# Performance work log

Measured on AMD Instinct MI355X. Metric: run time of the kernel, lower is better.

The kernel has to match this reference:

```python
import jax, jax.numpy as jnp
import numpy as np

N_HEADS = 16

def _rel_emb(table, len_q, len_k):
    # table: [2P+1, d] -> [len_q, len_k, d] via clipped relative distance lookup
    P = (table.shape[0] - 1) // 2
    rel = jnp.arange(len_k)[None, :] - jnp.arange(len_q)[:, None]
    idx = jnp.clip(rel, -P, P) + P
    return table[idx]

def setup_inputs() -> dict:
    key = jax.random.key(0)
    ks = jax.random.split(key, 13)
    B, S, E = 2, 2048, 1024
    P = 128
    d = E // N_HEADS
    s = 0.02
    return {
        "q": jax.random.normal(ks[0], (B, S, E), jnp.float32),
        "k": jax.random.normal(ks[1], (B, S, E), jnp.float32),
        "v": jax.random.normal(ks[2], (B, S, E), jnp.float32),
        "Wq": jax.random.normal(ks[3], (E, E), jnp.float32) * s,
        "bq": jnp.zeros((E,), jnp.float32),
        "Wk": jax.random.normal(ks[4], (E, E), jnp.float32) * s,
        "bk": jnp.zeros((E,), jnp.float32),
        "Wv": jax.random.normal(ks[5], (E, E), jnp.float32) * s,
        "bv": jnp.zeros((E,), jnp.float32),
        "Wo": jax.random.normal(ks[6], (E, E), jnp.float32) * s,
        "bo": jnp.zeros((E,), jnp.float32),
        "rk_table": jax.random.normal(ks[7], (2 * P + 1, d), jnp.float32) * s,
        "rv_table": jax.random.normal(ks[8], (2 * P + 1, d), jnp.float32) * s,
    }

def reference(q, k, v, Wq, bq, Wk, bk, Wv, bv, Wo, bo, rk_table, rv_table):
    B, Sq, E = q.shape
    Sk = k.shape[1]
    H = N_HEADS
    d = E // H
    scale = jnp.sqrt(jnp.asarray(d, q.dtype))

    qh = (q @ Wq.T + bq).reshape(B, Sq, H, d).transpose(0, 2, 1, 3)  # [B,H,Sq,d]
    kh = (k @ Wk.T + bk).reshape(B, Sk, H, d).transpose(0, 2, 1, 3)
    vh = (v @ Wv.T + bv).reshape(B, Sk, H, d).transpose(0, 2, 1, 3)

    qk = jnp.einsum('bhqd,bhkd->bhqk', qh, kh)
    r_k = _rel_emb(rk_table, Sq, Sk)                 # [Sq,Sk,d]
    q_rk = jnp.einsum('bhqd,qkd->bhqk', qh, r_k)
    attn = jax.nn.softmax((qk + q_rk) / scale, axis=-1)  # dropout p=0

    w1 = jnp.einsum('bhqk,bhkd->bhqd', attn, vh)
    r_v = _rel_emb(rv_table, Sq, Sk)
    w2 = jnp.einsum('bhqk,qkd->bhqd', attn, r_v)

    out = (w1 + w2).transpose(0, 2, 1, 3).reshape(B, Sq, E)
    return out @ Wo.T + bo
```

## Files before the change

### kernel.cpp

```cpp
#include <hip/hip_runtime.h>
#include <hip/hip_bf16.h>
#include <cstdint>
#include <cstddef>

#define NH   16
#define DH   64
#define SQ   2048
#define NB   2
#define EM   1024
#define NREL 257
#define QSTR 258
#define SCL  0.18033688f
#define NR   ((size_t)NB * NH * SQ)

typedef unsigned short ushort_t;
using bf16x8 = __attribute__((ext_vector_type(8))) __bf16;
using bf16x4 = __attribute__((ext_vector_type(4))) __bf16;
using f32x4  = __attribute__((ext_vector_type(4))) float;
#define MFMA16(a, b, c) __builtin_amdgcn_mfma_f32_16x16x32_bf16(a, b, c, 0, 0, 0)

__device__ __forceinline__ ushort_t f2bf(float f) {
    union { __bf16 h; ushort_t u; } x; x.h = (__bf16)f; return x.u;
}
__device__ __forceinline__ float bf2f(ushort_t u) {
    union { unsigned u; float f; } x; x.u = ((unsigned)u) << 16;
    return x.f;
}
__device__ __forceinline__ uint2 pack4(float a, float b, float c, float d) {
    union { bf16x4 v; uint2 u; } x;
    x.v = (bf16x4){ (__bf16)a, (__bf16)b, (__bf16)c, (__bf16)d };
    return x.u;
}
__device__ __forceinline__ int kperm(int x) {
    return (x & ~63) | ((x & 15) << 2) | ((x >> 4) & 3);
}
__device__ __forceinline__ void gl_lds16(const void* g, void* l) {
    __builtin_amdgcn_global_load_lds(
        (const __attribute__((address_space(1))) unsigned int*)g,
        (__attribute__((address_space(3))) unsigned int*)l, 16, 0, 0);
}

__global__ __launch_bounds__(256)
void cvt3(const float* __restrict__ a, const float* __restrict__ b,
          const float* __restrict__ c, ushort_t* __restrict__ oa,
          ushort_t* __restrict__ ob, ushort_t* __restrict__ oc, int n)
{
    const float* in = blockIdx.y == 0 ? a : (blockIdx.y == 1 ? b : c);
    ushort_t* out   = blockIdx.y == 0 ? oa : (blockIdx.y == 1 ? ob : oc);
    int i = (blockIdx.x * 256 + threadIdx.x) * 8;
    if (i < n) {
        float4 v0 = *reinterpret_cast<const float4*>(in + i);
        float4 v1 = *reinterpret_cast<const float4*>(in + i + 4);
        uint2 lo = pack4(v0.x, v0.y, v0.z, v0.w);
        uint2 hi = pack4(v1.x, v1.y, v1.z, v1.w);
        *reinterpret_cast<uint4*>(out + i) = make_uint4(lo.x, lo.y, hi.x, hi.y);
    }
}
__global__ __launch_bounds__(256)
void cvt4(const float* __restrict__ a, const float* __restrict__ b,
          const float* __restrict__ c, const float* __restrict__ d,
          ushort_t* __restrict__ oa, ushort_t* __restrict__ ob,
          ushort_t* __restrict__ oc, ushort_t* __restrict__ od, int n)
{
    const float* in = blockIdx.y == 0 ? a : (blockIdx.y == 1 ? b :
                      (blockIdx.y == 2 ? c : d));
    ushort_t* out   = blockIdx.y == 0 ? oa : (blockIdx.y == 1 ? ob :
                      (blockIdx.y == 2 ? oc : od));
    int i = (blockIdx.x * 256 + threadIdx.x) * 8;
    if (i < n) {
        float4 v0 = *reinterpret_cast<const float4*>(in + i);
        float4 v1 = *reinterpret_cast<const float4*>(in + i + 4);
        uint2 lo = pack4(v0.x, v0.y, v0.z, v0.w);
        uint2 hi = pack4(v1.x, v1.y, v1.z, v1.w);
        *reinterpret_cast<uint4*>(out + i) = make_uint4(lo.x, lo.y, hi.x, hi.y);
    }
}

__global__ __launch_bounds__(256)
void prep_tables(const float* __restrict__ rv, const float* __restrict__ rk,
                 ushort_t* __restrict__ rvT, ushort_t* __restrict__ rkb)
{
    int idx = blockIdx.x * 256 + threadIdx.x;
    if (idx < 64 * 256) {
        int d = idx >> 8, c = idx & 255;
        rvT[d * 256 + kperm(c)] = f2bf(rv[(size_t)(c + 1) * DH + d]);
    }
    idx -= 64 * 256;
    if (idx >= 0 && idx < 272 * 64) {
        int j = idx >> 6, d2 = idx & 63;
        rkb[idx] = (j < NREL) ? f2bf(rk[(size_t)j * DH + d2]) : (ushort_t)0;
    }
}

template<int MODE>
__global__ __launch_bounds__(256)
void gemm_bt(const ushort_t* __restrict__ A, const ushort_t* __restrict__ W,
             const float* __restrict__ bias, void* __restrict__ dstv,
             int M, int N, int K)
{
    __shared__ ushort_t As[128 * 32];
    __shared__ ushort_t Bs[128 * 32];
    const int t = threadIdx.x, lane = t & 63;
    const int wv = t >> 6, wr = wv >> 1, wc = wv & 1;
    const int g = lane >> 4, c16 = lane & 15;
    const int rowi = lane >> 2, chi = lane & 3;

    const int nwg = gridDim.x * gridDim.y;
    int flat = blockIdx.y * gridDim.x + blockIdx.x;
    int rm = (flat & 7) * (nwg >> 3) + (flat >> 3);
    const int n0 = (rm % gridDim.x) * 128;
    const int m0 = (rm / gridDim.x) * 128;

    f32x4 acc[4][4];
#pragma unroll
    for (int i = 0; i < 4; ++i)
#pragma unroll
        for (int j = 0; j < 4; ++j) acc[i][j] = (f32x4){0.f, 0.f, 0.f, 0.f};

    for (int k0 = 0; k0 < K; k0 += 32) {
        __syncthreads();
#pragma unroll
        for (int j = 0; j < 2; ++j) {
            const int rbase = wv * 32 + j * 16;
            gl_lds16(A + (size_t)(m0 + rbase + rowi) * K + k0 + chi * 8,
                     As + rbase * 32);
            gl_lds16(W + (size_t)(n0 + rbase + rowi) * K + k0 + chi * 8,
                     Bs + rbase * 32);
        }
        __syncthreads();

        bf16x8 af[4], bfr[4];
#pragma unroll
        for (int i = 0; i < 4; ++i)
            af[i] = *reinterpret_cast<const bf16x8*>(As + (wr * 64 + i * 16 + c16) * 32 + g * 8);
#pragma unroll
        for (int j = 0; j < 4; ++j)
            bfr[j] = *reinterpret_cast<const bf16x8*>(Bs + (wc * 64 + j * 16 + c16) * 32 + g * 8);
#pragma unroll
        for (int i = 0; i < 4; ++i)
#pragma unroll
            for (int j = 0; j < 4; ++j)
                acc[i][j] = MFMA16(af[i], bfr[j], acc[i][j]);
    }

#pragma unroll
    for (int j = 0; j < 4; ++j) {
        const int n = n0 + wc * 64 + j * 16 + c16;
        const float bn = bias[n];
#pragma unroll
        for (int i = 0; i < 4; ++i) {
#pragma unroll
            for (int r = 0; r < 4; ++r) {
                const int m = m0 + wr * 64 + i * 16 + 4 * g + r;
                const float vv = acc[i][j][r] + bn;
                if (MODE == 0) {
                    ((float*)dstv)[(size_t)m * N + n] = vv;
                } else {
                    const int b = m >> 11, s = m & (SQ - 1);
                    const int h = n >> 6, dd = n & 63;
                    if (MODE == 1) {
                        ((ushort_t*)dstv)[(((size_t)b * NH + h) * SQ + s) * DH + dd] = f2bf(vv);
                    } else {
                        const int sp = kperm(s);
                        ((ushort_t*)dstv)[(((size_t)b * NH + h) * DH + dd) * SQ + sp] = f2bf(vv);
                    }
                }
            }
        }
    }
}

__global__ __launch_bounds__(256)
void qrel_mfma(const ushort_t* __restrict__ qh, const ushort_t* __restrict__ rkb,
               ushort_t* __restrict__ qrel)
{
    const int t = threadIdx.x, lane = t & 63, w = t >> 6;
    const int g = lane >> 4, c16 = lane & 15;
    const size_t r0 = (size_t)blockIdx.x * 64 + w * 16;

    bf16x8 af[2];
#pragma unroll
    for (int ks = 0; ks < 2; ++ks)
        af[ks] = *reinterpret_cast<const bf16x8*>(qh + (r0 + c16) * DH + ks * 32 + g * 8);

    f32x4 acc[17];
#pragma unroll
    for (int n = 0; n < 17; ++n) acc[n] = (f32x4){0.f, 0.f, 0.f, 0.f};
#pragma unroll
    for (int n = 0; n < 17; ++n)
#pragma unroll
        for (int ks = 0; ks < 2; ++ks) {
            bf16x8 bf = *reinterpret_cast<const bf16x8*>(
                rkb + (size_t)(16 * n + c16) * DH + ks * 32 + g * 8);
            acc[n] = MFMA16(af[ks], bf, acc[n]);
        }
#pragma unroll
    for (int n = 0; n < 17; ++n) {
        const int j = 16 * n + c16;
        if (j < NREL) {
#pragma unroll
            for (int r = 0; r < 4; ++r)
                qrel[(r0 + 4 * g + r) * QSTR + j] = f2bf(acc[n][r] * SCL);
        }
    }
}

__global__ __launch_bounds__(256, 4)
void attn_flash(const ushort_t* __restrict__ qh, const ushort_t* __restrict__ kh,
                const ushort_t* __restrict__ vt, const ushort_t* __restrict__ qrel,
                ushort_t* __restrict__ Ptile, float* __restrict__ w1g,
                float* __restrict__ lacg, float* __restrict__ b0g,
                float* __restrict__ b256g)
{
    __shared__ ushort_t Ks[64 * 72];
    __shared__ ushort_t Vs[64 * 72];
    __shared__ ushort_t PQs[64 * 72];

    const int t = threadIdx.x, lane = t & 63, w = t >> 6;
    const int g = lane >> 4, c16 = lane & 15;
    const int nwg = gridDim.x * gridDim.y;
    int flat = blockIdx.y * gridDim.x + blockIdx.x;
    int rmid = (flat & 7) * (nwg >> 3) + (flat >> 3);
    const int q0 = (rmid & 31) * 64;
    const int bh = rmid >> 5;
    const size_t Gbase = ((size_t)bh * 32 + (q0 >> 6)) * 5;

#pragma unroll
    for (int l = 0; l < 2; ++l) {
        const int fid = t + 256 * l;
        const int row = fid >> 3, ch = fid & 7;
        uint4 v = *reinterpret_cast<const uint4*>(
            qh + ((size_t)bh * SQ + q0 + row) * DH + ch * 8);
        *reinterpret_cast<uint4*>(PQs + row * 72 + ch * 8) = v;
    }
    __syncthreads();
    bf16x8 qf[2];
#pragma unroll
    for (int ks = 0; ks < 2; ++ks)
        qf[ks] = *reinterpret_cast<const bf16x8*>(PQs + (w * 16 + c16) * 72 + ks * 32 + g * 8);

    const ushort_t* qrb = qrel + ((size_t)bh * SQ + q0) * QSTR;
    float q0add[4], q256add[4];
#pragma unroll
    for (int i = 0; i < 4; ++i) {
        const int r = w * 16 + 4 * g + i;
        q0add[i]   = bf2f(qrb[(size_t)r * QSTR + 0]);
        q256add[i] = bf2f(qrb[(size_t)r * QSTR + 256]);
    }

    f32x4 w1[4];
#pragma unroll
    for (int n = 0; n < 4; ++n) w1[n] = (f32x4){0.f, 0.f, 0.f, 0.f};
    float lac[4] = {0.f,0.f,0.f,0.f}, b0[4] = {0.f,0.f,0.f,0.f}, b256[4] = {0.f,0.f,0.f,0.f};

    const int row_l = t >> 3, ch_l = t & 7;
    const int row_h = row_l + 32;
    uint4 kr0, kr1, vr0, vr1;
    {
        kr0 = *reinterpret_cast<const uint4*>(kh + ((size_t)bh * SQ + row_l) * DH + ch_l * 8);
        kr1 = *reinterpret_cast<const uint4*>(kh + ((size_t)bh * SQ + row_h) * DH + ch_l * 8);
        vr0 = *reinterpret_cast<const uint4*>(vt + ((size_t)bh * DH + row_l) * SQ + ch_l * 8);
        vr1 = *reinterpret_cast<const uint4*>(vt + ((size_t)bh * DH + row_h) * SQ + ch_l * 8);
    }

    for (int k0 = 0; k0 < SQ; k0 += 64) {
        __syncthreads();
        *reinterpret_cast<uint4*>(Ks + row_l * 72 + ch_l * 8) = kr0;
        *reinterpret_cast<uint4*>(Ks + row_h * 72 + ch_l * 8) = kr1;
        *reinterpret_cast<uint4*>(Vs + row_l * 72 + ch_l * 8) = vr0;
        *reinterpret_cast<uint4*>(Vs + row_h * 72 + ch_l * 8) = vr1;
        __syncthreads();
        if (k0 + 64 < SQ) {
            kr0 = *reinterpret_cast<const uint4*>(kh + ((size_t)bh * SQ + k0 + 64 + row_l) * DH + ch_l * 8);
            kr1 = *reinterpret_cast<const uint4*>(kh + ((size_t)bh * SQ + k0 + 64 + row_h) * DH + ch_l * 8);
            vr0 = *reinterpret_cast<const uint4*>(vt + ((size_t)bh * DH + row_l) * SQ + k0 + 64 + ch_l * 8);
            vr1 = *reinterpret_cast<const uint4*>(vt + ((size_t)bh * DH + row_h) * SQ + k0 + 64 + ch_l * 8);
        }

        f32x4 s[4];
#pragma unroll
        for (int n = 0; n < 4; ++n) s[n] = (f32x4){0.f, 0.f, 0.f, 0.f};
        __builtin_amdgcn_s_setprio(1);
#pragma unroll
        for (int ks = 0; ks < 2; ++ks)
#pragma unroll
            for (int n = 0; n < 4; ++n) {
                bf16x8 kf = *reinterpret_cast<const bf16x8*>(
                    Ks + (16 * n + c16) * 72 + ks * 32 + g * 8);
                s[n] = MFMA16(qf[ks], kf, s[n]);
            }
        __builtin_amdgcn_s_setprio(0);

        const int rel0 = k0 - q0;
        float rsum[4] = {0.f, 0.f, 0.f, 0.f};
        if (rel0 <= -192 || rel0 >= 192) {
            const bool lo = rel0 < 0;
#pragma unroll
            for (int i = 0; i < 4; ++i) {
                const float add = lo ? q0add[i] : q256add[i];
#pragma unroll
                for (int n = 0; n < 4; ++n) {
                    const float p = exp2f(fmaf(s[n][i], SCL, add));
                    s[n][i] = p; rsum[i] += p;
                }
                if (lo) b0[i] += rsum[i]; else b256[i] += rsum[i];
                const int qloc = w * 16 + 4 * g + i;
                *reinterpret_cast<uint2*>(PQs + qloc * 72 + c16 * 4) =
                    pack4(s[0][i], s[1][i], s[2][i], s[3][i]);
            }
        } else if (rel0 == -128 || rel0 == 128) {
            const int tix = (rel0 + 128) >> 6;
#pragma unroll
            for (int i = 0; i < 4; ++i) {
                const int qloc = w * 16 + 4 * g + i;
                const ushort_t* qrow = qrb + (size_t)qloc * QSTR;
                float z[4];
#pragma unroll
                for (int n = 0; n < 4; ++n) {
                    const int rel = rel0 + 16 * n + c16 - qloc;
                    const int idx = rel < -128 ? 0 : (rel > 128 ? 256 : rel + 128);
                    const float p = exp2f(fmaf(s[n][i], SCL, bf2f(qrow[idx])));
                    s[n][i] = p; rsum[i] += p;
                    const bool inb = (rel >= -127) & (rel <= 127);
                    z[n] = inb ? p : 0.f;
                    if (rel <= -128)      b0[i] += p;
                    else if (rel >= 128)  b256[i] += p;
                }
                *reinterpret_cast<uint2*>(PQs + qloc * 72 + c16 * 4) =
                    pack4(s[0][i], s[1][i], s[2][i], s[3][i]);
                *reinterpret_cast<uint2*>(
                    Ptile + ((Gbase + tix) * 64 + qloc) * 64 + 4 * c16) =
                    pack4(z[0], z[1], z[2], z[3]);
            }
        } else {
            const int tix = (rel0 + 128) >> 6;
#pragma unroll
            for (int i = 0; i < 4; ++i) {
                const int qloc = w * 16 + 4 * g + i;
                const ushort_t* qrow = qrb + (size_t)qloc * QSTR;
#pragma unroll
                for (int n = 0; n < 4; ++n) {
                    const int rel = rel0 + 16 * n + c16 - qloc;
                    const float p = exp2f(fmaf(s[n][i], SCL, bf2f(qrow[rel + 128])));
                    s[n][i] = p; rsum[i] += p;
                }
                const uint2 pk = pack4(s[0][i], s[1][i], s[2][i], s[3][i]);
                *reinterpret_cast<uint2*>(PQs + qloc * 72 + c16 * 4) = pk;
                *reinterpret_cast<uint2*>(
                    Ptile + ((Gbase + tix) * 64 + qloc) * 64 + 4 * c16) = pk;
            }
        }
#pragma unroll
        for (int i = 0; i < 4; ++i) lac[i] += rsum[i];

        __builtin_amdgcn_s_setprio(1);
#pragma unroll
        for (int ks = 0; ks < 2; ++ks) {
            bf16x8 pf = *reinterpret_cast<const bf16x8*>(
                PQs + (w * 16 + c16) * 72 + ks * 32 + g * 8);
#pragma unroll
            for (int n = 0; n < 4; ++n) {
                bf16x8 vf = *reinterpret_cast<const bf16x8*>(
                    Vs + (16 * n + c16) * 72 + ks * 32 + g * 8);
                w1[n] = MFMA16(pf, vf, w1[n]);
            }
        }
        __builtin_amdgcn_s_setprio(0);
    }

#pragma unroll
    for (int m = 1; m < 16; m <<= 1)
#pragma unroll
        for (int i = 0; i < 4; ++i) {
            lac[i]  += __shfl_xor(lac[i],  m, 64);
            b0[i]   += __shfl_xor(b0[i],   m, 64);
            b256[i] += __shfl_xor(b256[i], m, 64);
        }
    if (c16 == 0) {
#pragma unroll
        for (int i = 0; i < 4; ++i) {
            const size_t row = (size_t)bh * SQ + q0 + w * 16 + 4 * g + i;
            lacg[row] = lac[i]; b0g[row] = b0[i]; b256g[row] = b256[i];
        }
    }
#pragma unroll
    for (int n = 0; n < 4; ++n)
#pragma unroll
        for (int i = 0; i < 4; ++i) {
            const size_t row = (size_t)bh * SQ + q0 + w * 16 + 4 * g + i;
            w1g[row * DH + 16 * n + c16] = w1[n][i];
        }
}

__global__ __launch_bounds__(256)
void band_gemm(const ushort_t* __restrict__ Ptile, const ushort_t* __restrict__ rvT,
               const float* __restrict__ rv_f32, const float* __restrict__ w1g,
               const float* __restrict__ lacg, const float* __restrict__ b0g,
               const float* __restrict__ b256g, ushort_t* __restrict__ wout)
{
    __shared__ ushort_t Pband[64 * 264];
    const int t = threadIdx.x, lane = t & 63, w = t >> 6;
    const int g = lane >> 4, c16 = lane & 15;
    const int G = blockIdx.x;
    const size_t r0 = (size_t)G * 64;
    const int q0 = (G & 31) * 64;

    for (int i = t; i < 64 * 264 / 2; i += 256)
        reinterpret_cast<unsigned*>(Pband)[i] = 0u;
    __syncthreads();

    for (int u = t; u < 5 * 64 * 16; u += 256) {
        const int tix = u >> 10;
        const int kt0 = q0 + (tix - 2) * 64;
        if (kt0 < 0 || kt0 >= SQ) continue;
        const int qloc = (u >> 4) & 63;
        const int c = u & 15;
        uint2 pv = *reinterpret_cast<const uint2*>(
            Ptile + (((size_t)G * 5 + tix) * 64 + qloc) * 64 + 4 * c);
        const ushort_t* pe = reinterpret_cast<const ushort_t*>(&pv);
        const int relbase = (tix - 2) * 64 - qloc + 127;
#pragma unroll
        for (int n = 0; n < 4; ++n) {
            const int x = relbase + 16 * n + c;
            if (x >= 0 && x <= 254)
                Pband[qloc * 264 + ((x & ~63) | ((x & 15) << 2) | ((x >> 4) & 3))] = pe[n];
        }
    }
    if (t < 64) Pband[t * 264 + 255] = f2bf(b256g[r0 + t]);
    __syncthreads();

    f32x4 acc[4];
#pragma unroll
    for (int n = 0; n < 4; ++n) acc[n] = (f32x4){0.f, 0.f, 0.f, 0.f};
#pragma unroll
    for (int ks = 0; ks < 8; ++ks) {
        bf16x8 pm = *reinterpret_cast<const bf16x8*>(
            Pband + (w * 16 + c16) * 264 + ks * 32 + g * 8);
#pragma unroll
        for (int n = 0; n < 4; ++n) {
            bf16x8 rf = *reinterpret_cast<const bf16x8*>(
                rvT + (size_t)(16 * n + c16) * 256 + ks * 32 + g * 8);
            acc[n] = MFMA16(pm, rf, acc[n]);
        }
    }

#pragma unroll
    for (int i = 0; i < 4; ++i) {
        const size_t row = r0 + w * 16 + 4 * g + i;
        const float inv = 1.0f / lacg[row];
        const float vb0 = b0g[row];
        const int b = (int)(row >> 15), h = (int)((row >> 11) & 15), s = (int)(row & 2047);
#pragma unroll
        for (int n = 0; n < 4; ++n) {
            const int col = 16 * n + c16;
            const float val = (w1g[row * DH + col] + acc[n][i] + vb0 * rv_f32[col]) * inv;
            wout[(((size_t)b * SQ + s) * NH + h) * DH + col] = f2bf(val);
        }
    }
}

extern "C" void kernel_launch(void* const* d_in, const int* in_sizes, int n_in,
                              void* d_out, int out_size, void* d_ws, size_t ws_size,
                              hipStream_t stream)
{
    const float* q  = (const float*)d_in[0];
    const float* k  = (const float*)d_in[1];
    const float* v  = (const float*)d_in[2];
    const float* Wq = (const float*)d_in[3];
    const float* bq = (const float*)d_in[4];
    const float* Wk = (const float*)d_in[5];
    const float* bk = (const float*)d_in[6];
    const float* Wv = (const float*)d_in[7];
    const float* bv = (const float*)d_in[8];
    const float* Wo = (const float*)d_in[9];
    const float* bo = (const float*)d_in[10];
    const float* rk = (const float*)d_in[11];
    const float* rv = (const float*)d_in[12];

    char* ws = (char*)d_ws;
    auto alloc = [&](size_t bytes) { char* p = ws; ws += bytes; return p; };
    const size_t QB = (size_t)NB * SQ * EM * 2;
    const size_t WB = (size_t)EM * EM * 2;

    char* region0 = alloc(NR * 320 * 2);
    ushort_t* Ptile = (ushort_t*)region0;
    ushort_t* qbf = (ushort_t*)region0;
    ushort_t* kbf = (ushort_t*)(region0 + QB);
    ushort_t* vbf = (ushort_t*)(region0 + 2 * QB);
    ushort_t* Wqb = (ushort_t*)(region0 + 3 * QB);
    ushort_t* Wkb = (ushort_t*)(region0 + 3 * QB + WB);
    ushort_t* Wvb = (ushort_t*)(region0 + 3 * QB + 2 * WB);

    ushort_t* Wob  = (ushort_t*)alloc(WB);
    ushort_t* qhb  = (ushort_t*)alloc(QB);
    ushort_t* khb  = (ushort_t*)alloc(QB);
    ushort_t* vtb  = (ushort_t*)alloc(QB);
    ushort_t* wbuf = (ushort_t*)alloc(QB);
    ushort_t* rvT  = (ushort_t*)alloc(64 * 256 * 2);
    ushort_t* rkb  = (ushort_t*)alloc(272 * 64 * 2);
    ushort_t* qrel = (ushort_t*)alloc(NR * QSTR * 2);
    float*    w1g  = (float*)alloc(NR * DH * 4);
    float*    lacg = (float*)alloc(NR * 4);
    float*    b0g  = (float*)alloc(NR * 4);
    float*    b256g= (float*)alloc(NR * 4);

    const int NQ = NB * SQ * EM;
    const int NW = EM * EM;
    cvt3<<<dim3(NQ / 2048, 3), 256, 0, stream>>>(q, k, v, qbf, kbf, vbf, NQ);
    cvt4<<<dim3(NW / 2048, 4), 256, 0, stream>>>(Wq, Wk, Wv, Wo, Wqb, Wkb, Wvb, Wob, NW);
    prep_tables<<<132, 256, 0, stream>>>(rv, rk, rvT, rkb);

    const int M = NB * SQ;
    dim3 gg(EM / 128, M / 128);
    gemm_bt<1><<<gg, 256, 0, stream>>>(qbf, Wqb, bq, qhb, M, EM, EM);
    gemm_bt<1><<<gg, 256, 0, stream>>>(kbf, Wkb, bk, khb, M, EM, EM);
    gemm_bt<2><<<gg, 256, 0, stream>>>(vbf, Wvb, bv, vtb, M, EM, EM);
    qrel_mfma<<<(int)(NR / 64), 256, 0, stream>>>(qhb, rkb, qrel);

    attn_flash<<<dim3(32, 32), 256, 0, stream>>>(qhb, khb, vtb, qrel,
                                                 Ptile, w1g, lacg, b0g, b256g);
    band_gemm<<<(int)(NR / 64), 256, 0, stream>>>(Ptile, rvT, rv, w1g, lacg,
                                                  b0g, b256g, wbuf);
    gemm_bt<0><<<gg, 256, 0, stream>>>(wbuf, Wob, bo, d_out, M, EM, EM);
}
```

Before: 282.5 us.

## Fuse band GEMM epilogue into flash attention and halve GEMM N-tile

The relative-value band GEMM and the final normalization now run inside the attention kernel, reusing its shared memory for the band tile. The w1, row-sum and boundary-sum values stay in registers instead of going to global memory and being read back by a separate kernel, which also saves a launch. The projection GEMMs switch from 128x128 to 128x64 tiles, doubling the grid to improve CU fill. In exchange, attention blocks need more LDS and registers, which may reduce occupancy, and the smaller GEMM tiles reuse each loaded A tile less.

```diff
diff --git a/kernel.cpp b/kernel.cpp
--- a/kernel.cpp
+++ b/kernel.cpp
@@ -99,7 +99,7 @@
              int M, int N, int K)
 {
     __shared__ ushort_t As[128 * 32];
-    __shared__ ushort_t Bs[128 * 32];
+    __shared__ ushort_t Bs[64 * 32];
     const int t = threadIdx.x, lane = t & 63;
     const int wv = t >> 6, wr = wv >> 1, wc = wv & 1;
     const int g = lane >> 4, c16 = lane & 15;
@@ -108,14 +108,14 @@
     const int nwg = gridDim.x * gridDim.y;
     int flat = blockIdx.y * gridDim.x + blockIdx.x;
     int rm = (flat & 7) * (nwg >> 3) + (flat >> 3);
-    const int n0 = (rm % gridDim.x) * 128;
+    const int n0 = (rm % gridDim.x) * 64;
     const int m0 = (rm / gridDim.x) * 128;
 
-    f32x4 acc[4][4];
+    f32x4 acc[4][2];
 #pragma unroll
     for (int i = 0; i < 4; ++i)
 #pragma unroll
-        for (int j = 0; j < 4; ++j) acc[i][j] = (f32x4){0.f, 0.f, 0.f, 0.f};
+        for (int j = 0; j < 2; ++j) acc[i][j] = (f32x4){0.f, 0.f, 0.f, 0.f};
 
     for (int k0 = 0; k0 < K; k0 += 32) {
         __syncthreads();
@@ -124,28 +124,31 @@
             const int rbase = wv * 32 + j * 16;
             gl_lds16(A + (size_t)(m0 + rbase + rowi) * K + k0 + chi * 8,
                      As + rbase * 32);
+        }
+        {
+            const int rbase = wv * 16;
             gl_lds16(W + (size_t)(n0 + rbase + rowi) * K + k0 + chi * 8,
                      Bs + rbase * 32);
         }
         __syncthreads();
 
-        bf16x8 af[4], bfr[4];
+        bf16x8 af[4], bfr[2];
 #pragma unroll
         for (int i = 0; i < 4; ++i)
             af[i] = *reinterpret_cast<const bf16x8*>(As + (wr * 64 + i * 16 + c16) * 32 + g * 8);
 #pragma unroll
-        for (int j = 0; j < 4; ++j)
-            bfr[j] = *reinterpret_cast<const bf16x8*>(Bs + (wc * 64 + j * 16 + c16) * 32 + g * 8);
+        for (int j = 0; j < 2; ++j)
+            bfr[j] = *reinterpret_cast<const bf16x8*>(Bs + (wc * 32 + j * 16 + c16) * 32 + g * 8);
 #pragma unroll
         for (int i = 0; i < 4; ++i)
 #pragma unroll
-            for (int j = 0; j < 4; ++j)
+            for (int j = 0; j < 2; ++j)
                 acc[i][j] = MFMA16(af[i], bfr[j], acc[i][j]);
     }
 
 #pragma unroll
-    for (int j = 0; j < 4; ++j) {
-        const int n = n0 + wc * 64 + j * 16 + c16;
+    for (int j = 0; j < 2; ++j) {
+        const int n = n0 + wc * 32 + j * 16 + c16;
         const float bn = bias[n];
 #pragma unroll
         for (int i = 0; i < 4; ++i) {
@@ -208,13 +211,14 @@
 __global__ __launch_bounds__(256, 4)
 void attn_flash(const ushort_t* __restrict__ qh, const ushort_t* __restrict__ kh,
                 const ushort_t* __restrict__ vt, const ushort_t* __restrict__ qrel,
-                ushort_t* __restrict__ Ptile, float* __restrict__ w1g,
-                float* __restrict__ lacg, float* __restrict__ b0g,
-                float* __restrict__ b256g)
-{
-    __shared__ ushort_t Ks[64 * 72];
-    __shared__ ushort_t Vs[64 * 72];
-    __shared__ ushort_t PQs[64 * 72];
+                const ushort_t* __restrict__ rvT, const float* __restrict__ rv_f32,
+                ushort_t* __restrict__ Ptile, ushort_t* __restrict__ wout)
+{
+    __shared__ ushort_t SM[64 * 264];
+    ushort_t* Ks  = SM;
+    ushort_t* Vs  = SM + 4608;
+    ushort_t* PQs = SM + 9216;
+    ushort_t* Pband = SM;
 
     const int t = threadIdx.x, lane = t & 63, w = t >> 6;
     const int g = lane >> 4, c16 = lane & 15;
@@ -223,7 +227,7 @@
     int rmid = (flat & 7) * (nwg >> 3) + (flat >> 3);
     const int q0 = (rmid & 31) * 64;
     const int bh = rmid >> 5;
-    const size_t Gbase = ((size_t)bh * 32 + (q0 >> 6)) * 5;
+    const size_t Gbase = (size_t)rmid * 5;
 
 #pragma unroll
     for (int l = 0; l < 2; ++l) {
@@ -376,35 +380,8 @@
             b0[i]   += __shfl_xor(b0[i],   m, 64);
             b256[i] += __shfl_xor(b256[i], m, 64);
         }
-    if (c16 == 0) {
-#pragma unroll
-        for (int i = 0; i < 4; ++i) {
-            const size_t row = (size_t)bh * SQ + q0 + w * 16 + 4 * g + i;
-            lacg[row] = lac[i]; b0g[row] = b0[i]; b256g[row] = b256[i];
-        }
-    }
-#pragma unroll
-    for (int n = 0; n < 4; ++n)
-#pragma unroll
-        for (int i = 0; i < 4; ++i) {
-            const size_t row = (size_t)bh * SQ + q0 + w * 16 + 4 * g + i;
-            w1g[row * DH + 16 * n + c16] = w1[n][i];
-        }
-}
-
-__global__ __launch_bounds__(256)
-void band_gemm(const ushort_t* __restrict__ Ptile, const ushort_t* __restrict__ rvT,
-               const float* __restrict__ rv_f32, const float* __restrict__ w1g,
-               const float* __restrict__ lacg, const float* __restrict__ b0g,
-               const float* __restrict__ b256g, ushort_t* __restrict__ wout)
-{
-    __shared__ ushort_t Pband[64 * 264];
-    const int t = threadIdx.x, lane = t & 63, w = t >> 6;
-    const int g = lane >> 4, c16 = lane & 15;
-    const int G = blockIdx.x;
-    const size_t r0 = (size_t)G * 64;
-    const int q0 = (G & 31) * 64;
-
+
+    __syncthreads();
     for (int i = t; i < 64 * 264 / 2; i += 256)
         reinterpret_cast<unsigned*>(Pband)[i] = 0u;
     __syncthreads();
@@ -416,7 +393,7 @@
         const int qloc = (u >> 4) & 63;
         const int c = u & 15;
         uint2 pv = *reinterpret_cast<const uint2*>(
-            Ptile + (((size_t)G * 5 + tix) * 64 + qloc) * 64 + 4 * c);
+            Ptile + ((Gbase + tix) * 64 + qloc) * 64 + 4 * c);
         const ushort_t* pe = reinterpret_cast<const ushort_t*>(&pv);
         const int relbase = (tix - 2) * 64 - qloc + 127;
 #pragma unroll
@@ -426,12 +403,16 @@
                 Pband[qloc * 264 + ((x & ~63) | ((x & 15) << 2) | ((x >> 4) & 3))] = pe[n];
         }
     }
-    if (t < 64) Pband[t * 264 + 255] = f2bf(b256g[r0 + t]);
+    if (c16 == 0) {
+#pragma unroll
+        for (int i = 0; i < 4; ++i)
+            Pband[(w * 16 + 4 * g + i) * 264 + 255] = f2bf(b256[i]);
+    }
     __syncthreads();
 
-    f32x4 acc[4];
-#pragma unroll
-    for (int n = 0; n < 4; ++n) acc[n] = (f32x4){0.f, 0.f, 0.f, 0.f};
+    f32x4 w2a[4];
+#pragma unroll
+    for (int n = 0; n < 4; ++n) w2a[n] = (f32x4){0.f, 0.f, 0.f, 0.f};
 #pragma unroll
     for (int ks = 0; ks < 8; ++ks) {
         bf16x8 pm = *reinterpret_cast<const bf16x8*>(
@@ -440,21 +421,21 @@
         for (int n = 0; n < 4; ++n) {
             bf16x8 rf = *reinterpret_cast<const bf16x8*>(
                 rvT + (size_t)(16 * n + c16) * 256 + ks * 32 + g * 8);
-            acc[n] = MFMA16(pm, rf, acc[n]);
-        }
-    }
-
+            w2a[n] = MFMA16(pm, rf, w2a[n]);
+        }
+    }
+
+    const int b = bh >> 4, hh = bh & 15;
 #pragma unroll
     for (int i = 0; i < 4; ++i) {
-        const size_t row = r0 + w * 16 + 4 * g + i;
-        const float inv = 1.0f / lacg[row];
-        const float vb0 = b0g[row];
-        const int b = (int)(row >> 15), h = (int)((row >> 11) & 15), s = (int)(row & 2047);
+        const int qg = q0 + w * 16 + 4 * g + i;
+        const float inv = 1.0f / lac[i];
+        const float vb0 = b0[i];
 #pragma unroll
         for (int n = 0; n < 4; ++n) {
             const int col = 16 * n + c16;
-            const float val = (w1g[row * DH + col] + acc[n][i] + vb0 * rv_f32[col]) * inv;
-            wout[(((size_t)b * SQ + s) * NH + h) * DH + col] = f2bf(val);
+            const float val = (w1[n][i] + w2a[n][i] + vb0 * rv_f32[col]) * inv;
+            wout[(((size_t)b * SQ + qg) * NH + hh) * DH + col] = f2bf(val);
         }
     }
 }
@@ -499,10 +480,6 @@
     ushort_t* rvT  = (ushort_t*)alloc(64 * 256 * 2);
     ushort_t* rkb  = (ushort_t*)alloc(272 * 64 * 2);
     ushort_t* qrel = (ushort_t*)alloc(NR * QSTR * 2);
-    float*    w1g  = (float*)alloc(NR * DH * 4);
-    float*    lacg = (float*)alloc(NR * 4);
-    float*    b0g  = (float*)alloc(NR * 4);
-    float*    b256g= (float*)alloc(NR * 4);
 
     const int NQ = NB * SQ * EM;
     const int NW = EM * EM;
@@ -511,15 +488,13 @@
     prep_tables<<<132, 256, 0, stream>>>(rv, rk, rvT, rkb);
 
     const int M = NB * SQ;
-    dim3 gg(EM / 128, M / 128);
+    dim3 gg(EM / 64, M / 128);
     gemm_bt<1><<<gg, 256, 0, stream>>>(qbf, Wqb, bq, qhb, M, EM, EM);
     gemm_bt<1><<<gg, 256, 0, stream>>>(kbf, Wkb, bk, khb, M, EM, EM);
     gemm_bt<2><<<gg, 256, 0, stream>>>(vbf, Wvb, bv, vtb, M, EM, EM);
     qrel_mfma<<<(int)(NR / 64), 256, 0, stream>>>(qhb, rkb, qrel);
 
     attn_flash<<<dim3(32, 32), 256, 0, stream>>>(qhb, khb, vtb, qrel,
-                                                 Ptile, w1g, lacg, b0g, b256g);
-    band_gemm<<<(int)(NR / 64), 256, 0, stream>>>(Ptile, rvT, rv, w1g, lacg,
-                                                  b0g, b256g, wbuf);
-    gemm_bt<0><<<gg, 256, 0, stream>>>(wbuf, Wob, bo, d_out, M, EM, EM);
-}
+                                                 rvT, rv, Ptile, wbuf);
+    gemm_bt<0><<<gg, 256, 0, stream>>>(wbuf, Wob, bo, (float*)d_out, M, EM, EM);
+}
```

Measured after the change: 269.6 us. 4.6% less time.
